# Kernel tuning notes

Hardware: AMD Instinct MI355X
Metric: run time of the kernel (lower is better)

## Reference

```python
import jax, jax.numpy as jnp
import numpy as np

EMBED = 2048
NUM_EXPERTS = 64
TOP_K = 8


def setup_inputs() -> dict:
    key = jax.random.key(0)
    k1, k2, k3 = jax.random.split(key, 3)
    inputs = jax.random.normal(k1, (8, 4096, EMBED), dtype=jnp.float32)
    # nn.Linear(embed_size, num_experts): weight [num_experts, embed_size], bias [num_experts]
    W = jax.random.normal(k2, (NUM_EXPERTS, EMBED), dtype=jnp.float32) / np.sqrt(EMBED)
    b = jax.random.normal(k3, (NUM_EXPERTS,), dtype=jnp.float32) * 0.01
    return {"inputs": inputs, "W": W, "b": b}


def reference(inputs, W, b):
    # Linear projection: [B, S, E] x [E, N] -> [B, S, N]
    logits = jnp.einsum('bse,ne->bsn', inputs, W) + b
    # top-k selection along expert axis
    _, indices = jax.lax.top_k(logits, TOP_K)  # [B, S, K] int32
    # scatter mask: 1 at selected experts (one_hot sum == scatter_ of ones)
    mask = jax.nn.one_hot(indices, NUM_EXPERTS, dtype=jnp.bool_).any(axis=-2)  # [B, S, N]
    # masked_fill(-inf) + softmax -> probs only on selected experts
    masked = jnp.where(mask, logits, -jnp.inf)
    probs = jax.nn.softmax(masked, axis=-1)
    return probs, indices
```

## Files before the change

### kernel.cpp

```cpp
#include <hip/hip_runtime.h>
#include <cmath>

#define NTOK 32768
#define EMB  2048
#define NEXP 64
#define TOPK 8
#define BT   64
#define KC   64
#define NCH  (EMB / KC)

typedef __attribute__((ext_vector_type(4))) double d4;

__device__ __forceinline__ void gld16(const float* g, float* lds) {
    __builtin_amdgcn_global_load_lds(
        (const __attribute__((address_space(1))) void*)g,
        (__attribute__((address_space(3))) void*)lds,
        16, 0, 0);
}

__global__ __launch_bounds__(256) void router_mfma(
    const float* __restrict__ X,
    const float* __restrict__ W,
    const float* __restrict__ Bv,
    float* __restrict__ out)
{
    __shared__ float xs[2][BT * KC];
    __shared__ float ws[2][NEXP * KC];

    const int tid  = threadIdx.x;
    const int lane = tid & 63;
    const int wv   = tid >> 6;
    const int t0   = blockIdx.x * BT;
    const int eL   = lane & 15;
    const int q    = lane >> 4;
    const int sw   = 4 * (eL & 7);

    d4 acc[4];
    #pragma unroll
    for (int c = 0; c < 4; ++c) {
        const double b = (double)Bv[c * 16 + eL];
        acc[c] = (d4){b, b, b, b};
    }

    auto stage = [&](int ch, int buf) {
        const int kc0 = ch * KC;
        #pragma unroll
        for (int s = 0; s < 4; ++s) {
            const int i  = 4 * wv + s;
            const int r  = 4 * i + (lane >> 4);
            const int ag = (lane & 15) ^ (r & 7);
            gld16(&X[(size_t)(t0 + r) * EMB + kc0 + 4 * ag], &xs[buf][i * 256]);
            gld16(&W[(size_t)r * EMB + kc0 + 4 * ag], &ws[buf][i * 256]);
        }
    };

    stage(0, 0);
    __syncthreads();

    for (int ch = 0; ch < NCH; ++ch) {
        const int cur = ch & 1;
        if (ch + 1 < NCH) stage(ch + 1, cur ^ 1);

        const float* xb = &xs[cur][(wv * 16 + eL) * KC];
        const float* wb = ws[cur];
        #pragma unroll
        for (int k4 = 0; k4 < KC; k4 += 4) {
            const int kk = (k4 + q) ^ sw;
            const double aF = (double)xb[kk];
            #pragma unroll
            for (int c = 0; c < 4; ++c) {
                const double bF = (double)wb[(c * 16 + eL) * KC + kk];
                acc[c] = __builtin_amdgcn_mfma_f64_16x16x4f64(aF, bF, acc[c], 0, 0, 0);
            }
        }
        __syncthreads();
    }

    float* probs = out;
    float* idxo  = out + (size_t)NTOK * NEXP;

    #pragma unroll
    for (int i = 0; i < 4; ++i) {
        const int T = t0 + wv * 16 + q + 4 * i;
        double v[4];
        #pragma unroll
        for (int c = 0; c < 4; ++c) v[c] = acc[c][i];

        unsigned sel = 0;
        double m0 = 0.0;
        float ssum = 0.0f;
        int myIdx = 0;
        #pragma unroll
        for (int it = 0; it < TOPK; ++it) {
            double bv = -1.0e300;
            int    be = 1 << 30;
            #pragma unroll
            for (int c = 0; c < 4; ++c)
                if (!((sel >> c) & 1) && v[c] > bv) { bv = v[c]; be = c * 16 + eL; }
            double gv = bv; int ge = be;
            #pragma unroll
            for (int off = 1; off <= 8; off <<= 1) {
                const double ov = __shfl_xor(gv, off, 64);
                const int    oe = __shfl_xor(ge, off, 64);
                if (ov > gv || (ov == gv && oe < ge)) { gv = ov; ge = oe; }
            }
            if (it == 0) m0 = gv;
            ssum += __expf((float)(gv - m0));
            if ((ge & 15) == eL) sel |= 1u << (ge >> 4);
            if (eL == it) myIdx = ge;
        }
        const float inv = 1.0f / ssum;
        #pragma unroll
        for (int c = 0; c < 4; ++c) {
            const float p = ((sel >> c) & 1) ? __expf((float)(v[c] - m0)) * inv : 0.0f;
            probs[(size_t)T * NEXP + c * 16 + eL] = p;
        }
        if (eL < TOPK) idxo[(size_t)T * TOPK + eL] = (float)myIdx;
    }
}

extern "C" void kernel_launch(void* const* d_in, const int* in_sizes, int n_in,
                              void* d_out, int out_size, void* d_ws, size_t ws_size,
                              hipStream_t stream) {
    const float* X = (const float*)d_in[0];
    const float* W = (const float*)d_in[1];
    const float* B = (const float*)d_in[2];
    router_mfma<<<NTOK / BT, 256, 0, stream>>>(X, W, B, (float*)d_out);
}
```

Before: 462.9 us.

## Split K dimension across two wave groups with LDS partial-sum reduction

```diff
diff --git a/kernel.cpp b/kernel.cpp
--- a/kernel.cpp
+++ b/kernel.cpp
@@ -6,8 +6,10 @@
 #define NEXP 64
 #define TOPK 8
 #define BT   64
-#define KC   64
-#define NCH  (EMB / KC)
+#define KC   32
+#define KGN  2
+#define KSPAN (EMB / KGN)
+#define NCH  (KSPAN / KC)
 
 typedef __attribute__((ext_vector_type(4))) double d4;
 
@@ -18,18 +20,20 @@
         16, 0, 0);
 }
 
-__global__ __launch_bounds__(256) void router_mfma(
+__global__ __launch_bounds__(512) void router_mfma(
     const float* __restrict__ X,
     const float* __restrict__ W,
     const float* __restrict__ Bv,
     float* __restrict__ out)
 {
-    __shared__ float xs[2][BT * KC];
-    __shared__ float ws[2][NEXP * KC];
+    __shared__ __align__(16) float xs[KGN][2][BT * KC];
+    __shared__ __align__(16) float ws[KGN][2][NEXP * KC];
 
     const int tid  = threadIdx.x;
     const int lane = tid & 63;
     const int wv   = tid >> 6;
+    const int tt   = wv & 3;
+    const int kg   = wv >> 2;
     const int t0   = blockIdx.x * BT;
     const int eL   = lane & 15;
     const int q    = lane >> 4;
@@ -38,19 +42,19 @@
     d4 acc[4];
     #pragma unroll
     for (int c = 0; c < 4; ++c) {
-        const double b = (double)Bv[c * 16 + eL];
+        const double b = (kg == 0) ? (double)Bv[c * 16 + eL] : 0.0;
         acc[c] = (d4){b, b, b, b};
     }
 
     auto stage = [&](int ch, int buf) {
-        const int kc0 = ch * KC;
+        const int kc0 = kg * KSPAN + ch * KC;
         #pragma unroll
-        for (int s = 0; s < 4; ++s) {
-            const int i  = 4 * wv + s;
-            const int r  = 4 * i + (lane >> 4);
-            const int ag = (lane & 15) ^ (r & 7);
-            gld16(&X[(size_t)(t0 + r) * EMB + kc0 + 4 * ag], &xs[buf][i * 256]);
-            gld16(&W[(size_t)r * EMB + kc0 + 4 * ag], &ws[buf][i * 256]);
+        for (int s = 0; s < 2; ++s) {
+            const int i  = 2 * tt + s;
+            const int r  = 8 * i + (lane >> 3);
+            const int ag = (lane & 7) ^ (lane >> 3);
+            gld16(&X[(size_t)(t0 + r) * EMB + kc0 + 4 * ag], &xs[kg][buf][i * 256]);
+            gld16(&W[(size_t)r * EMB + kc0 + 4 * ag], &ws[kg][buf][i * 256]);
         }
     };
 
@@ -61,8 +65,8 @@
         const int cur = ch & 1;
         if (ch + 1 < NCH) stage(ch + 1, cur ^ 1);
 
-        const float* xb = &xs[cur][(wv * 16 + eL) * KC];
-        const float* wb = ws[cur];
+        const float* xb = &xs[kg][cur][(tt * 16 + eL) * KC];
+        const float* wb = ws[kg][cur];
         #pragma unroll
         for (int k4 = 0; k4 < KC; k4 += 4) {
             const int kk = (k4 + q) ^ sw;
@@ -76,12 +80,29 @@
         __syncthreads();
     }
 
+    double* part = (double*)xs;
+    if (kg == 1) {
+        #pragma unroll
+        for (int c = 0; c < 4; ++c)
+            #pragma unroll
+            for (int i = 0; i < 4; ++i)
+                part[(size_t)(tt * 16 + c * 4 + i) * 64 + lane] = acc[c][i];
+    }
+    __syncthreads();
+    if (kg == 1) return;
+
+    #pragma unroll
+    for (int c = 0; c < 4; ++c)
+        #pragma unroll
+        for (int i = 0; i < 4; ++i)
+            acc[c][i] += part[(size_t)(tt * 16 + c * 4 + i) * 64 + lane];
+
     float* probs = out;
     float* idxo  = out + (size_t)NTOK * NEXP;
 
     #pragma unroll
     for (int i = 0; i < 4; ++i) {
-        const int T = t0 + wv * 16 + q + 4 * i;
+        const int T = t0 + tt * 16 + q + 4 * i;
         double v[4];
         #pragma unroll
         for (int c = 0; c < 4; ++c) v[c] = acc[c][i];
@@ -125,5 +146,5 @@
     const float* X = (const float*)d_in[0];
     const float* W = (const float*)d_in[1];
     const float* B = (const float*)d_in[2];
-    router_mfma<<<NTOK / BT, 256, 0, stream>>>(X, W, B, (float*)d_out);
+    router_mfma<<<NTOK / BT, 512, 0, stream>>>(X, W, B, (float*)d_out);
 }
```

New measurement: 454.5 us. No clear change (-1.8%).
